# Kernel optimization log

Measured on AMD Instinct MI355X. Metric: run time of the kernel, lower is better.

## Reference

```python
import jax, jax.numpy as jnp
import numpy as np

B, N, H = 16, 1024, 4
CH = (64, 128, 256, 512)
KV = 960
EPS = 1e-5  # InstanceNorm2d default eps


def setup_inputs() -> dict:
    key = jax.random.key(0)
    ks = jax.random.split(key, 16)
    s = 0.02
    inp = {
        "emb1": jax.random.normal(ks[0], (B, N, CH[0]), jnp.float32),
        "emb2": jax.random.normal(ks[1], (B, N, CH[1]), jnp.float32),
        "emb3": jax.random.normal(ks[2], (B, N, CH[2]), jnp.float32),
        "emb4": jax.random.normal(ks[3], (B, N, CH[3]), jnp.float32),
        "emb_all": jax.random.normal(ks[4], (B, N, KV), jnp.float32),
        # per-head query weights (torch Linear weight layout [out, in])
        "Wq1": jax.random.normal(ks[5], (H, CH[0] // 4, CH[0] // 4), jnp.float32) * s,
        "Wq2": jax.random.normal(ks[6], (H, CH[1] // 4, CH[1] // 4), jnp.float32) * s,
        "Wq3": jax.random.normal(ks[7], (H, CH[2] // 4, CH[2] // 4), jnp.float32) * s,
        "Wq4": jax.random.normal(ks[8], (H, CH[3] // 4, CH[3] // 4), jnp.float32) * s,
        # NOTE: original forward only ever uses self.key[0] / self.value[0]
        "Wk": jax.random.normal(ks[9], (KV // 4, KV // 4), jnp.float32) * s,
        "Wv": jax.random.normal(ks[10], (KV // 4, KV // 4), jnp.float32) * s,
        "Wo1": jax.random.normal(ks[11], (CH[0], CH[0]), jnp.float32) * s,
        "Wo2": jax.random.normal(ks[12], (CH[1], CH[1]), jnp.float32) * s,
        "Wo3": jax.random.normal(ks[13], (CH[2], CH[2]), jnp.float32) * s,
        "Wo4": jax.random.normal(ks[14], (CH[3], CH[3]), jnp.float32) * s,
    }
    return inp


def _heads_from_all(x):
    # Reproduce the per-head channel regrouping of emb_all:
    # head h takes [16h:16(h+1)] of scale1, [32h:...] of scale2, etc. -> [B,H,N,240]
    b, n, _ = x.shape
    parts = [
        x[:, :, 0:64].reshape(b, n, H, 16),
        x[:, :, 64:192].reshape(b, n, H, 32),
        x[:, :, 192:448].reshape(b, n, H, 64),
        x[:, :, 448:960].reshape(b, n, H, 128),
    ]
    return jnp.concatenate(parts, axis=-1).transpose(0, 2, 1, 3)


def _scale_attn(emb, Wq, Wo, Kh, Vh):
    b, n, c = emb.shape
    d = c // H
    q = emb.reshape(b, n, H, d)
    # per-head linear (torch: x @ W.T): [B,H,N,d]
    Qh = jnp.einsum('bnhd,hed->bhne', q, Wq)
    # channel attention: Q^T K -> [B,H,d,240]
    scores = jnp.einsum('bhnd,bhnk->bhdk', Qh, Kh) / np.float32(np.sqrt(KV))
    # InstanceNorm2d over heads (per (b,h), normalize over last two dims, biased var)
    m = scores.mean(axis=(2, 3), keepdims=True)
    v = scores.var(axis=(2, 3), keepdims=True)
    probs = jax.nn.softmax((scores - m) / jnp.sqrt(v + EPS), axis=-1)
    # probs @ V^T -> [B,H,d,N]
    ctx = jnp.einsum('bhdk,bhnk->bhdn', probs, Vh)
    # permute(0,3,2,1) -> [B,N,d,H], flatten -> [B,N,c]
    ctx = ctx.transpose(0, 3, 2, 1).reshape(b, n, c)
    return jnp.einsum('bnc,ec->bne', ctx, Wo)


def reference(emb1, emb2, emb3, emb4, emb_all,
              Wq1, Wq2, Wq3, Wq4, Wk, Wv, Wo1, Wo2, Wo3, Wo4):
    heads = _heads_from_all(emb_all)  # [B,H,N,240]
    Kh = jnp.einsum('bhnd,ed->bhne', heads, Wk)
    Vh = jnp.einsum('bhnd,ed->bhne', heads, Wv)
    O1 = _scale_attn(emb1, Wq1, Wo1, Kh, Vh)
    O2 = _scale_attn(emb2, Wq2, Wo2, Kh, Vh)
    O3 = _scale_attn(emb3, Wq3, Wo3, Kh, Vh)
    O4 = _scale_attn(emb4, Wq4, Wo4, Kh, Vh)
    return (O1, O2, O3, O4)
```

## Files before the change

kernel.cpp:

```cpp
#include <hip/hip_runtime.h>
#include <hip/hip_bf16.h>
#include <math.h>

#define B_   16
#define N_   1024
#define H_   4
#define D240 240
#define SC_  57600

typedef unsigned short ushort;
typedef __attribute__((ext_vector_type(8))) short bf16x8;
typedef __attribute__((ext_vector_type(8))) unsigned short u16x8;
typedef __attribute__((ext_vector_type(4))) float f32x4;

__device__ __forceinline__ ushort f2b(float v) {
  __hip_bfloat16 h = __float2bfloat16(v);
  return *reinterpret_cast<ushort*>(&h);
}

__device__ __forceinline__ void gload16(const void* g, void* s) {
  __builtin_amdgcn_global_load_lds((const __attribute__((address_space(1))) void*)g,
                                   (__attribute__((address_space(3))) void*)s, 16, 0, 0);
}

__global__ __launch_bounds__(256) void conv_inputs(const float* __restrict__ emb_all,
                                                   const float* __restrict__ e1,
                                                   const float* __restrict__ e2,
                                                   const float* __restrict__ e3,
                                                   const float* __restrict__ e4,
                                                   ushort* __restrict__ heads,
                                                   ushort* __restrict__ embh) {
  const int t = threadIdx.x;
  const int which = t >> 7;
  const int gg = t & 127;
  const int h = gg >> 5;
  const int k0 = (gg & 31) * 8;
  const bool active = (k0 < 240);

  const float* base;
  int stride;
  long soff;
  if (which == 0) {
    base = emb_all; stride = 960;
    if (k0 < 16)       soff = h * 16 + k0;
    else if (k0 < 48)  soff = 64  + h * 32  + (k0 - 16);
    else if (k0 < 112) soff = 192 + h * 64  + (k0 - 48);
    else               soff = 448 + h * 128 + (k0 - 112);
  } else {
    if (k0 < 16)       { base = e1; stride = 64;  soff = h * 16  + k0; }
    else if (k0 < 48)  { base = e2; stride = 128; soff = h * 32  + (k0 - 16); }
    else if (k0 < 112) { base = e3; stride = 256; soff = h * 64  + (k0 - 48); }
    else               { base = e4; stride = 512; soff = h * 128 + (k0 - 112); }
  }
  ushort* dbase = which ? embh : heads;

  #pragma unroll
  for (int i = 0; i < 8; ++i) {
    const int bn = blockIdx.x * 8 + i;
    const int b = bn >> 10, n = bn & 1023;
    float4 p0 = {0.f, 0.f, 0.f, 0.f}, p1 = {0.f, 0.f, 0.f, 0.f};
    if (active) {
      const float* s = base + (long)bn * stride + soff;
      p0 = *(const float4*)s;
      p1 = *(const float4*)(s + 4);
    }
    u16x8 w;
    w[0] = f2b(p0.x); w[1] = f2b(p0.y); w[2] = f2b(p0.z); w[3] = f2b(p0.w);
    w[4] = f2b(p1.x); w[5] = f2b(p1.y); w[6] = f2b(p1.z); w[7] = f2b(p1.w);
    *(u16x8*)(dbase + (((long)b * H_ + h) * N_ + n) * 256 + k0) = w;
  }
}

__global__ __launch_bounds__(256) void conv_weights(
    const float* __restrict__ Wk, const float* __restrict__ Wv,
    const float* __restrict__ q1, const float* __restrict__ q2,
    const float* __restrict__ q3, const float* __restrict__ q4,
    const float* __restrict__ o1, const float* __restrict__ o2,
    const float* __restrict__ o3, const float* __restrict__ o4,
    ushort* __restrict__ wts) {
  long i = (long)blockIdx.x * 256 + threadIdx.x;
  if (i >= 716800) return;
  float v = 0.f;
  if (i < 122880) {
    const float* src = (i < 61440) ? Wk : Wv;
    long j = (i < 61440) ? i : i - 61440;
    int r = j / 256, k = j % 256;
    if (k < 240) v = src[(long)r * 240 + k];
  } else if (i < 368640) {
    long j = i - 122880;
    int h = j / 61440; int rem = j % 61440;
    int r = rem / 256, k = rem % 256;
    int s = r < 16 ? 0 : r < 48 ? 1 : r < 112 ? 2 : 3;
    const int dss[4] = {16, 32, 64, 128};
    const int qf[4]  = {0, 16, 48, 112};
    const float* qs[4] = {q1, q2, q3, q4};
    int d = dss[s], off = qf[s];
    if (k >= off && k < off + d)
      v = qs[s][((long)(h * d + (r - off))) * d + (k - off)];
  } else {
    long j = i - 368640;
    int s = j < 4096 ? 0 : j < 20480 ? 1 : j < 86016 ? 2 : 3;
    const long base[4] = {0, 4096, 20480, 86016};
    const int cs[4] = {64, 128, 256, 512};
    const float* os[4] = {o1, o2, o3, o4};
    long rem = j - base[s];
    int c = cs[s], d = c >> 2;
    int e = rem / c, kk = rem % c;
    v = os[s][(long)e * c + (kk % d) * 4 + kk / d];
  }
  wts[i] = f2b(v);
}

__device__ __forceinline__ void gemm_core_b16(
    ushort* As, ushort* Bs,
    const ushort* __restrict__ A, long lda,
    const ushort* __restrict__ Bm, long ldb,
    ushort* __restrict__ C, long ldc,
    int M, int Nn, int Npad, int K, int m0, int n0)
{
  const int tid = threadIdx.x;
  const int l = tid & 63, w = tid >> 6;
  const int wy = w >> 1, wx = w & 1;

  f32x4 acc[4][4];
  #pragma unroll
  for (int i = 0; i < 4; ++i)
    #pragma unroll
    for (int j = 0; j < 4; ++j) acc[i][j] = (f32x4)0.f;

  const int srow = tid >> 2;
  const int skc  = (tid & 3) * 8;
  int ra0 = m0 + srow;      ra0 = ra0 < M  ? ra0 : M - 1;
  int ra1 = m0 + srow + 64; ra1 = ra1 < M  ? ra1 : M - 1;
  int rb0 = n0 + srow;      rb0 = rb0 < Nn ? rb0 : Nn - 1;
  int rb1 = n0 + srow + 64; rb1 = rb1 < Nn ? rb1 : Nn - 1;
  const ushort* a0 = A  + (long)ra0 * lda + skc;
  const ushort* a1 = A  + (long)ra1 * lda + skc;
  const ushort* b0 = Bm + (long)rb0 * ldb + skc;
  const ushort* b1 = Bm + (long)rb1 * ldb + skc;
  ushort* lA0 = As + srow * 32 + skc;
  ushort* lA1 = As + (srow + 64) * 32 + skc;
  ushort* lB0 = Bs + srow * 32 + skc;
  ushort* lB1 = Bs + (srow + 64) * 32 + skc;

  const ushort* arp = As + (wy * 64 + (l & 15)) * 32 + (l >> 4) * 8;
  const ushort* brp = Bs + (wx * 64 + (l & 15)) * 32 + (l >> 4) * 8;

  for (int k0 = 0; k0 < K; k0 += 32) {
    __syncthreads();
    gload16(a0 + k0, lA0);
    gload16(a1 + k0, lA1);
    gload16(b0 + k0, lB0);
    gload16(b1 + k0, lB1);
    __syncthreads();
    bf16x8 af[4], bfr[4];
    #pragma unroll
    for (int i = 0; i < 4; ++i) af[i]  = *(const bf16x8*)(arp + i * 512);
    #pragma unroll
    for (int j = 0; j < 4; ++j) bfr[j] = *(const bf16x8*)(brp + j * 512);
    #pragma unroll
    for (int i = 0; i < 4; ++i)
      #pragma unroll
      for (int j = 0; j < 4; ++j)
        acc[i][j] = __builtin_amdgcn_mfma_f32_16x16x32_bf16(af[i], bfr[j], acc[i][j], 0, 0, 0);
  }

  const int quad = l >> 4, lc = l & 15;
  #pragma unroll
  for (int i = 0; i < 4; ++i) {
    #pragma unroll
    for (int r = 0; r < 4; ++r) {
      int row = m0 + wy * 64 + i * 16 + quad * 4 + r;
      if (row >= M) continue;
      ushort* Cr = C + (long)row * ldc;
      #pragma unroll
      for (int j = 0; j < 4; ++j) {
        int col = n0 + wx * 64 + j * 16 + lc;
        if (col < Nn) Cr[col] = f2b(acc[i][j][r]);
        else if (col < Npad) Cr[col] = 0;
      }
    }
  }
}

__global__ __launch_bounds__(256) void mfma_proj(
    const ushort* __restrict__ heads_b, const ushort* __restrict__ emb_h,
    const ushort* __restrict__ Wk_b, const ushort* __restrict__ Wv_b,
    const ushort* __restrict__ Wq_bd,
    ushort* __restrict__ Kh_T, ushort* __restrict__ Vh, ushort* __restrict__ Q_T)
{
  __shared__ __align__(16) ushort As[128 * 32];
  __shared__ __align__(16) ushort Bs[128 * 32];
  const int bx = blockIdx.x;
  const long sbh = 1024L * 256;

  if (bx < 1024) {
    const int bh = bx >> 4, t = bx & 15;
    gemm_core_b16(As, Bs,
                  Wk_b, 256,
                  heads_b + (long)bh * sbh, 256,
                  Kh_T + (long)bh * 240 * 1024, 1024,
                  240, 1024, 1024, 256, (t >> 3) * 128, (t & 7) * 128);
  } else if (bx < 2048) {
    const int local = bx - 1024;
    const int bh = local >> 4, t = local & 15;
    gemm_core_b16(As, Bs,
                  heads_b + (long)bh * sbh, 256,
                  Wv_b, 256,
                  Vh + (long)bh * sbh, 256,
                  1024, 240, 256, 256, (t >> 1) * 128, (t & 1) * 128);
  } else {
    const int local = bx - 2048;
    const int bh = local >> 4, t = local & 15;
    const int h = bh & 3;
    gemm_core_b16(As, Bs,
                  Wq_bd + h * 61440, 256,
                  emb_h + (long)bh * sbh, 256,
                  Q_T + (long)bh * 240 * 1024, 1024,
                  240, 1024, 1024, 256, (t >> 3) * 128, (t & 7) * 128);
  }
}

__global__ __launch_bounds__(256) void mfma_abT(
    const ushort* __restrict__ A, long lda, long AsY, long AsZ,
    const ushort* __restrict__ Bm, long ldb, long BsY, long BsZ,
    void* __restrict__ Cv, long ldc, long CsY, long CsZ,
    int M, int Nn, int Npad, int K, float alpha, int c_bf16, int tilesN)
{
  A  += blockIdx.y * AsY + blockIdx.z * AsZ;
  Bm += blockIdx.y * BsY + blockIdx.z * BsZ;

  const int m0 = (blockIdx.x / tilesN) * 128;
  const int n0 = (blockIdx.x % tilesN) * 128;
  const int tid = threadIdx.x;
  const int l = tid & 63, w = tid >> 6;
  const int wy = w >> 1, wx = w & 1;

  __shared__ __align__(16) ushort As[128 * 32];
  __shared__ __align__(16) ushort Bs[128 * 32];

  f32x4 acc[4][4];
  #pragma unroll
  for (int i = 0; i < 4; ++i)
    #pragma unroll
    for (int j = 0; j < 4; ++j) acc[i][j] = (f32x4)0.f;

  const int srow = tid >> 2;
  const int skc  = (tid & 3) * 8;
  int ra0 = m0 + srow;      ra0 = ra0 < M  ? ra0 : M - 1;
  int ra1 = m0 + srow + 64; ra1 = ra1 < M  ? ra1 : M - 1;
  int rb0 = n0 + srow;      rb0 = rb0 < Nn ? rb0 : Nn - 1;
  int rb1 = n0 + srow + 64; rb1 = rb1 < Nn ? rb1 : Nn - 1;
  const ushort* a0 = A  + (long)ra0 * lda + skc;
  const ushort* a1 = A  + (long)ra1 * lda + skc;
  const ushort* b0 = Bm + (long)rb0 * ldb + skc;
  const ushort* b1 = Bm + (long)rb1 * ldb + skc;
  ushort* lA0 = As + srow * 32 + skc;
  ushort* lA1 = As + (srow + 64) * 32 + skc;
  ushort* lB0 = Bs + srow * 32 + skc;
  ushort* lB1 = Bs + (srow + 64) * 32 + skc;

  const ushort* arp = As + (wy * 64 + (l & 15)) * 32 + (l >> 4) * 8;
  const ushort* brp = Bs + (wx * 64 + (l & 15)) * 32 + (l >> 4) * 8;

  for (int k0 = 0; k0 < K; k0 += 32) {
    __syncthreads();
    gload16(a0 + k0, lA0);
    gload16(a1 + k0, lA1);
    gload16(b0 + k0, lB0);
    gload16(b1 + k0, lB1);
    __syncthreads();
    bf16x8 af[4], bfr[4];
    #pragma unroll
    for (int i = 0; i < 4; ++i) af[i]  = *(const bf16x8*)(arp + i * 512);
    #pragma unroll
    for (int j = 0; j < 4; ++j) bfr[j] = *(const bf16x8*)(brp + j * 512);
    #pragma unroll
    for (int i = 0; i < 4; ++i)
      #pragma unroll
      for (int j = 0; j < 4; ++j)
        acc[i][j] = __builtin_amdgcn_mfma_f32_16x16x32_bf16(af[i], bfr[j], acc[i][j], 0, 0, 0);
  }

  const int quad = l >> 4, lc = l & 15;
  if (c_bf16) {
    ushort* C = (ushort*)Cv + blockIdx.y * CsY + blockIdx.z * CsZ;
    #pragma unroll
    for (int i = 0; i < 4; ++i) {
      #pragma unroll
      for (int r = 0; r < 4; ++r) {
        int row = m0 + wy * 64 + i * 16 + quad * 4 + r;
        if (row >= M) continue;
        ushort* Cr = C + (long)row * ldc;
        #pragma unroll
        for (int j = 0; j < 4; ++j) {
          int col = n0 + wx * 64 + j * 16 + lc;
          if (col < Nn) Cr[col] = f2b(acc[i][j][r] * alpha);
          else if (col < Npad) Cr[col] = 0;
        }
      }
    }
  } else {
    float* C = (float*)Cv + blockIdx.y * CsY + blockIdx.z * CsZ;
    #pragma unroll
    for (int i = 0; i < 4; ++i) {
      #pragma unroll
      for (int r = 0; r < 4; ++r) {
        int row = m0 + wy * 64 + i * 16 + quad * 4 + r;
        if (row >= M) continue;
        float* Cr = C + (long)row * ldc;
        #pragma unroll
        for (int j = 0; j < 4; ++j) {
          int col = n0 + wx * 64 + j * 16 + lc;
          if (col < Nn) Cr[col] = acc[i][j][r] * alpha;
        }
      }
    }
  }
}

__global__ __launch_bounds__(256) void mfma_ctx(const ushort* __restrict__ V,
                                                const ushort* __restrict__ P,
                                                ushort* __restrict__ ctx2) {
  const int h = blockIdx.y, b = blockIdx.z;
  const ushort* A  = V + (((long)b * H_ + h) * 1024) * 256;
  const ushort* Bm = P + (((long)b * H_ + h) * 240) * 256;

  const int m0 = (blockIdx.x >> 1) * 128;
  const int n0 = (blockIdx.x & 1) * 128;
  const int tid = threadIdx.x;
  const int l = tid & 63, w = tid >> 6;
  const int wy = w >> 1, wx = w & 1;

  __shared__ __align__(16) ushort As[128 * 32];
  __shared__ __align__(16) ushort Bs[128 * 32];

  f32x4 acc[4][4];
  #pragma unroll
  for (int i = 0; i < 4; ++i)
    #pragma unroll
    for (int j = 0; j < 4; ++j) acc[i][j] = (f32x4)0.f;

  const int srow = tid >> 2;
  const int skc  = (tid & 3) * 8;
  int rb0 = n0 + srow;      rb0 = rb0 < 240 ? rb0 : 239;
  int rb1 = n0 + srow + 64; rb1 = rb1 < 240 ? rb1 : 239;
  const ushort* a0 = A  + (long)(m0 + srow) * 256 + skc;
  const ushort* a1 = A  + (long)(m0 + srow + 64) * 256 + skc;
  const ushort* b0 = Bm + (long)rb0 * 256 + skc;
  const ushort* b1 = Bm + (long)rb1 * 256 + skc;
  ushort* lA0 = As + srow * 32 + skc;
  ushort* lA1 = As + (srow + 64) * 32 + skc;
  ushort* lB0 = Bs + srow * 32 + skc;
  ushort* lB1 = Bs + (srow + 64) * 32 + skc;

  const ushort* arp = As + (wy * 64 + (l & 15)) * 32 + (l >> 4) * 8;
  const ushort* brp = Bs + (wx * 64 + (l & 15)) * 32 + (l >> 4) * 8;

  for (int k0 = 0; k0 < 256; k0 += 32) {
    __syncthreads();
    gload16(a0 + k0, lA0);
    gload16(a1 + k0, lA1);
    gload16(b0 + k0, lB0);
    gload16(b1 + k0, lB1);
    __syncthreads();
    bf16x8 af[4], bfr[4];
    #pragma unroll
    for (int i = 0; i < 4; ++i) af[i]  = *(const bf16x8*)(arp + i * 512);
    #pragma unroll
    for (int j = 0; j < 4; ++j) bfr[j] = *(const bf16x8*)(brp + j * 512);
    #pragma unroll
    for (int i = 0; i < 4; ++i)
      #pragma unroll
      for (int j = 0; j < 4; ++j)
        acc[i][j] = __builtin_amdgcn_mfma_f32_16x16x32_bf16(af[i], bfr[j], acc[i][j], 0, 0, 0);
  }

  const int quad = l >> 4, lc = l & 15;
  const int dss[4] = {16, 32, 64, 128};
  const int qf[4]  = {0, 16, 48, 112};
  const int cf[4]  = {0, 64, 192, 448};
  #pragma unroll
  for (int i = 0; i < 4; ++i) {
    #pragma unroll
    for (int r = 0; r < 4; ++r) {
      int row = m0 + wy * 64 + i * 16 + quad * 4 + r;
      ushort* Cr = ctx2 + ((long)b * N_ + row) * 960;
      #pragma unroll
      for (int j = 0; j < 4; ++j) {
        int col = n0 + wx * 64 + j * 16 + lc;
        if (col < 240) {
          int s = col < 16 ? 0 : col < 48 ? 1 : col < 112 ? 2 : 3;
          int chan = cf[s] + h * dss[s] + (col - qf[s]);
          Cr[chan] = f2b(acc[i][j][r]);
        }
      }
    }
  }
}

__global__ __launch_bounds__(256) void mfma_oproj(const ushort* __restrict__ ctx2,
                                                  const ushort* __restrict__ Wo_b,
                                                  float* __restrict__ out) {
  const int bx = blockIdx.x;
  int s = bx < 128 ? 0 : bx < 256 ? 1 : bx < 512 ? 2 : 3;
  const int sbase[4] = {0, 128, 256, 512};
  const int cs_[4]   = {64, 128, 256, 512};
  const int coff_[4] = {0, 64, 192, 448};
  const int wo_[4]   = {0, 4096, 20480, 86016};
  const long oo_[4]  = {0, 1048576, 3145728, 7340032};
  const int c = cs_[s];
  const int nt = (c + 127) >> 7;
  const int local = bx - sbase[s];
  const int m0 = (local / nt) * 128;
  const int n0 = (local % nt) * 128;

  const ushort* A  = ctx2 + coff_[s];
  const ushort* Bm = Wo_b + wo_[s];
  float* C = out + oo_[s];
  const int K = c, Nn = c;

  const int tid = threadIdx.x;
  const int l = tid & 63, w = tid >> 6;
  const int wy = w >> 1, wx = w & 1;

  __shared__ __align__(16) ushort As[128 * 32];
  __shared__ __align__(16) ushort Bs[128 * 32];

  f32x4 acc[4][4];
  #pragma unroll
  for (int i = 0; i < 4; ++i)
    #pragma unroll
    for (int j = 0; j < 4; ++j) acc[i][j] = (f32x4)0.f;

  const int srow = tid >> 2;
  const int skc  = (tid & 3) * 8;
  int rb0 = n0 + srow;      rb0 = rb0 < Nn ? rb0 : Nn - 1;
  int rb1 = n0 + srow + 64; rb1 = rb1 < Nn ? rb1 : Nn - 1;
  const ushort* a0 = A  + (long)(m0 + srow) * 960 + skc;
  const ushort* a1 = A  + (long)(m0 + srow + 64) * 960 + skc;
  const ushort* b0 = Bm + (long)rb0 * c + skc;
  const ushort* b1 = Bm + (long)rb1 * c + skc;
  ushort* lA0 = As + srow * 32 + skc;
  ushort* lA1 = As + (srow + 64) * 32 + skc;
  ushort* lB0 = Bs + srow * 32 + skc;
  ushort* lB1 = Bs + (srow + 64) * 32 + skc;

  const ushort* arp = As + (wy * 64 + (l & 15)) * 32 + (l >> 4) * 8;
  const ushort* brp = Bs + (wx * 64 + (l & 15)) * 32 + (l >> 4) * 8;

  for (int k0 = 0; k0 < K; k0 += 32) {
    __syncthreads();
    gload16(a0 + k0, lA0);
    gload16(a1 + k0, lA1);
    gload16(b0 + k0, lB0);
    gload16(b1 + k0, lB1);
    __syncthreads();
    bf16x8 af[4], bfr[4];
    #pragma unroll
    for (int i = 0; i < 4; ++i) af[i]  = *(const bf16x8*)(arp + i * 512);
    #pragma unroll
    for (int j = 0; j < 4; ++j) bfr[j] = *(const bf16x8*)(brp + j * 512);
    #pragma unroll
    for (int i = 0; i < 4; ++i)
      #pragma unroll
      for (int j = 0; j < 4; ++j)
        acc[i][j] = __builtin_amdgcn_mfma_f32_16x16x32_bf16(af[i], bfr[j], acc[i][j], 0, 0, 0);
  }

  const int quad = l >> 4, lc = l & 15;
  #pragma unroll
  for (int i = 0; i < 4; ++i) {
    #pragma unroll
    for (int r = 0; r < 4; ++r) {
      int row = m0 + wy * 64 + i * 16 + quad * 4 + r;
      float* Cr = C + (long)row * c;
      #pragma unroll
      for (int j = 0; j < 4; ++j) {
        int col = n0 + wx * 64 + j * 16 + lc;
        if (col < Nn) Cr[col] = acc[i][j][r];
      }
    }
  }
}

__global__ __launch_bounds__(256) void in_stats(const float* __restrict__ sc0,
                                                const float* __restrict__ sc1,
                                                float* __restrict__ stats) {
  const int doffs[4] = {0, 16, 48, 112};
  const int dss[4]   = {16, 32, 64, 128};
  const int bh = blockIdx.x, sidx = blockIdx.y;
  const long base = (long)bh * SC_ + doffs[sidx] * D240;
  const float4* A4 = (const float4*)(sc0 + base);
  const float4* B4 = (const float4*)(sc1 + base);
  const int n4 = dss[sidx] * 60;

  float s = 0.f, s2 = 0.f;
  for (int i = threadIdx.x; i < n4; i += 256) {
    float4 a = A4[i], b = B4[i];
    float x0 = a.x + b.x, x1 = a.y + b.y, x2 = a.z + b.z, x3 = a.w + b.w;
    s  += x0 + x1 + x2 + x3;
    s2 += x0 * x0 + x1 * x1 + x2 * x2 + x3 * x3;
  }
  #pragma unroll
  for (int o = 32; o > 0; o >>= 1) { s += __shfl_down(s, o); s2 += __shfl_down(s2, o); }

  __shared__ float wsum[4], wsum2[4];
  const int wave = threadIdx.x >> 6, lane = threadIdx.x & 63;
  if (lane == 0) { wsum[wave] = s; wsum2[wave] = s2; }
  __syncthreads();
  if (threadIdx.x == 0) {
    float n = (float)(n4 * 4);
    float ts = wsum[0] + wsum[1] + wsum[2] + wsum[3];
    float ts2 = wsum2[0] + wsum2[1] + wsum2[2] + wsum2[3];
    float mean = ts / n;
    float var = ts2 / n - mean * mean;
    stats[(bh * 4 + sidx) * 2]     = mean;
    stats[(bh * 4 + sidx) * 2 + 1] = rsqrtf(var + 1e-5f);
  }
}

__global__ __launch_bounds__(256) void sm_apply(const float* __restrict__ sc0,
                                                const float* __restrict__ sc1,
                                                const float* __restrict__ stats,
                                                ushort* __restrict__ P) {
  const int bh = blockIdx.y;
  const int row = blockIdx.x * 4 + (threadIdx.x >> 6);
  const int lane = threadIdx.x & 63;
  const int s = row < 16 ? 0 : row < 48 ? 1 : row < 112 ? 2 : 3;
  const float mean = stats[(bh * 4 + s) * 2];
  const float rstd = stats[(bh * 4 + s) * 2 + 1];
  const long base = (long)bh * SC_ + (long)row * D240;
  const float* r0 = sc0 + base;
  const float* r1 = sc1 + base;
  ushort* p = P + ((long)bh * D240 + row) * 256;

  float v[4];
  float mx = -1e30f;
  #pragma unroll
  for (int j = 0; j < 4; ++j) {
    int c = lane + j * 64;
    v[j] = (c < D240) ? (r0[c] + r1[c] - mean) * rstd : -1e30f;
    mx = fmaxf(mx, v[j]);
  }
  #pragma unroll
  for (int o = 32; o > 0; o >>= 1) mx = fmaxf(mx, __shfl_xor(mx, o));
  float sum = 0.f;
  #pragma unroll
  for (int j = 0; j < 4; ++j) {
    int c = lane + j * 64;
    v[j] = (c < D240) ? __expf(v[j] - mx) : 0.f;
    sum += v[j];
  }
  #pragma unroll
  for (int o = 32; o > 0; o >>= 1) sum += __shfl_xor(sum, o);
  float inv = 1.f / sum;
  #pragma unroll
  for (int j = 0; j < 4; ++j) {
    int c = lane + j * 64;
    p[c] = (c < D240) ? f2b(v[j] * inv) : (ushort)0;
  }
}

extern "C" void kernel_launch(void* const* d_in, const int* in_sizes, int n_in,
                              void* d_out, int out_size, void* d_ws, size_t ws_size,
                              hipStream_t stream) {
  const float* emb[4] = {(const float*)d_in[0], (const float*)d_in[1],
                         (const float*)d_in[2], (const float*)d_in[3]};
  const float* emb_all = (const float*)d_in[4];
  const float* Wq[4] = {(const float*)d_in[5], (const float*)d_in[6],
                        (const float*)d_in[7], (const float*)d_in[8]};
  const float* Wk = (const float*)d_in[9];
  const float* Wv = (const float*)d_in[10];
  const float* Wo[4] = {(const float*)d_in[11], (const float*)d_in[12],
                        (const float*)d_in[13], (const float*)d_in[14]};
  float* out = (float*)d_out;
  float* sc0 = (float*)d_out;
  float* sc1 = (float*)d_out + 64L * SC_;

  ushort* wsb     = (ushort*)d_ws;
  ushort* heads_b = wsb;
  ushort* ctx2    = wsb;
  ushort* emb_h   = wsb + 16777216;
  ushort* P_b     = wsb + 16777216;
  ushort* Q_T     = wsb + 33554432;
  ushort* Kh_T    = wsb + 49283072;
  ushort* Vh      = wsb + 65011712;
  ushort* wts     = wsb + 81788928;
  ushort* Wk_b  = wts;
  ushort* Wv_b  = wts + 61440;
  ushort* Wq_bd = wts + 122880;
  ushort* Wo_b  = wts + 368640;
  float*  stats = (float*)(wsb + 82505728);

  const float alpha_s = 1.0f / sqrtf(960.0f);

  conv_weights<<<dim3(2800), 256, 0, stream>>>(Wk, Wv, Wq[0], Wq[1], Wq[2], Wq[3],
                                               Wo[0], Wo[1], Wo[2], Wo[3], wts);
  conv_inputs<<<dim3(2048), 256, 0, stream>>>(emb_all, emb[0], emb[1], emb[2], emb[3],
                                              heads_b, emb_h);

  mfma_proj<<<dim3(3072), 256, 0, stream>>>(heads_b, emb_h, Wk_b, Wv_b, Wq_bd,
                                            Kh_T, Vh, Q_T);

  mfma_abT<<<dim3(4, 64, 2), 256, 0, stream>>>(
      Q_T, 1024, 240L * 1024, 512,
      Kh_T, 1024, 240L * 1024, 512,
      sc0, 240, (long)SC_, 64L * SC_,
      240, 240, 240, 512, alpha_s, 0, 2);

  in_stats<<<dim3(64, 4), 256, 0, stream>>>(sc0, sc1, stats);
  sm_apply<<<dim3(60, 64), 256, 0, stream>>>(sc0, sc1, stats, P_b);

  mfma_ctx<<<dim3(16, H_, B_), 256, 0, stream>>>(Vh, P_b, ctx2);

  mfma_oproj<<<dim3(1024), 256, 0, stream>>>(ctx2, Wo_b, out);
}
```

Measured before the change: 349.7 us.

## Fuse fp32-to-bf16 input conversion and head regrouping into projection GEMM

Removes the separate conv_inputs kernel and its bf16 staging buffers. The projection GEMM now reads fp32 activations directly, applies the per-head channel gather, converts to bf16 in registers and writes the result into LDS, prefetching the next k-slice into registers. This saves a full write and read of the staged bf16 inputs and one launch. In exchange, emb_all is now read and converted twice (for K and V) and once per tile column, and the loads are strided fp32 instead of async LDS loads.

Result: no change. 346.8 us (-0.8%).

```diff
diff --git a/kernel.cpp b/kernel.cpp
--- a/kernel.cpp
+++ b/kernel.cpp
@@ -23,52 +23,11 @@
                                    (__attribute__((address_space(3))) void*)s, 16, 0, 0);
 }
 
-__global__ __launch_bounds__(256) void conv_inputs(const float* __restrict__ emb_all,
-                                                   const float* __restrict__ e1,
-                                                   const float* __restrict__ e2,
-                                                   const float* __restrict__ e3,
-                                                   const float* __restrict__ e4,
-                                                   ushort* __restrict__ heads,
-                                                   ushort* __restrict__ embh) {
-  const int t = threadIdx.x;
-  const int which = t >> 7;
-  const int gg = t & 127;
-  const int h = gg >> 5;
-  const int k0 = (gg & 31) * 8;
-  const bool active = (k0 < 240);
-
-  const float* base;
-  int stride;
-  long soff;
-  if (which == 0) {
-    base = emb_all; stride = 960;
-    if (k0 < 16)       soff = h * 16 + k0;
-    else if (k0 < 48)  soff = 64  + h * 32  + (k0 - 16);
-    else if (k0 < 112) soff = 192 + h * 64  + (k0 - 48);
-    else               soff = 448 + h * 128 + (k0 - 112);
-  } else {
-    if (k0 < 16)       { base = e1; stride = 64;  soff = h * 16  + k0; }
-    else if (k0 < 48)  { base = e2; stride = 128; soff = h * 32  + (k0 - 16); }
-    else if (k0 < 112) { base = e3; stride = 256; soff = h * 64  + (k0 - 48); }
-    else               { base = e4; stride = 512; soff = h * 128 + (k0 - 112); }
-  }
-  ushort* dbase = which ? embh : heads;
-
-  #pragma unroll
-  for (int i = 0; i < 8; ++i) {
-    const int bn = blockIdx.x * 8 + i;
-    const int b = bn >> 10, n = bn & 1023;
-    float4 p0 = {0.f, 0.f, 0.f, 0.f}, p1 = {0.f, 0.f, 0.f, 0.f};
-    if (active) {
-      const float* s = base + (long)bn * stride + soff;
-      p0 = *(const float4*)s;
-      p1 = *(const float4*)(s + 4);
-    }
-    u16x8 w;
-    w[0] = f2b(p0.x); w[1] = f2b(p0.y); w[2] = f2b(p0.z); w[3] = f2b(p0.w);
-    w[4] = f2b(p1.x); w[5] = f2b(p1.y); w[6] = f2b(p1.z); w[7] = f2b(p1.w);
-    *(u16x8*)(dbase + (((long)b * H_ + h) * N_ + n) * 256 + k0) = w;
-  }
+__device__ __forceinline__ u16x8 cvt8(float4 a, float4 b) {
+  u16x8 w;
+  w[0] = f2b(a.x); w[1] = f2b(a.y); w[2] = f2b(a.z); w[3] = f2b(a.w);
+  w[4] = f2b(b.x); w[5] = f2b(b.y); w[6] = f2b(b.z); w[7] = f2b(b.w);
+  return w;
 }
 
 __global__ __launch_bounds__(256) void conv_weights(
@@ -111,47 +70,105 @@
   wts[i] = f2b(v);
 }
 
-__device__ __forceinline__ void gemm_core_b16(
-    ushort* As, ushort* Bs,
-    const ushort* __restrict__ A, long lda,
-    const ushort* __restrict__ Bm, long ldb,
-    ushort* __restrict__ C, long ldc,
-    int M, int Nn, int Npad, int K, int m0, int n0)
+__global__ __launch_bounds__(256) void mfma_proj(
+    const float* __restrict__ emb_all,
+    const float* __restrict__ e1, const float* __restrict__ e2,
+    const float* __restrict__ e3, const float* __restrict__ e4,
+    const ushort* __restrict__ Wk_b, const ushort* __restrict__ Wv_b,
+    const ushort* __restrict__ Wq_bd,
+    ushort* __restrict__ Kh_T, ushort* __restrict__ Vh, ushort* __restrict__ Q_T)
 {
+  __shared__ __align__(16) ushort As[128 * 32];
+  __shared__ __align__(16) ushort Bs[128 * 32];
+
+  const int bx = blockIdx.x;
+  const int mode = bx < 1024 ? 0 : bx < 2048 ? 1 : 2;
+  const int local = bx - (mode == 0 ? 0 : mode == 1 ? 1024 : 2048);
+  const int bh = local >> 4, t16 = local & 15;
+  const int b = bh >> 2, h = bh & 3;
+
+  int m0, n0;
+  const ushort* W;
+  ushort* C; long ldc; int M, Nn, Npad;
+  if (mode == 0) {
+    m0 = (t16 >> 3) * 128; n0 = (t16 & 7) * 128;
+    W = Wk_b; C = Kh_T + (long)bh * 240 * 1024; ldc = 1024;
+    M = 240; Nn = 1024; Npad = 1024;
+  } else if (mode == 1) {
+    m0 = (t16 >> 1) * 128; n0 = (t16 & 1) * 128;
+    W = Wv_b; C = Vh + (long)bh * 1024 * 256; ldc = 256;
+    M = 1024; Nn = 240; Npad = 256;
+  } else {
+    m0 = (t16 >> 3) * 128; n0 = (t16 & 7) * 128;
+    W = Wq_bd + h * 61440; C = Q_T + (long)bh * 240 * 1024; ldc = 1024;
+    M = 240; Nn = 1024; Npad = 1024;
+  }
+  const bool wa = (mode != 1);
+  const int wbase = wa ? m0 : n0;
+  const int cbase = wa ? n0 : m0;
+
   const int tid = threadIdx.x;
   const int l = tid & 63, w = tid >> 6;
   const int wy = w >> 1, wx = w & 1;
-
-  f32x4 acc[4][4];
-  #pragma unroll
-  for (int i = 0; i < 4; ++i)
-    #pragma unroll
-    for (int j = 0; j < 4; ++j) acc[i][j] = (f32x4)0.f;
-
   const int srow = tid >> 2;
   const int skc  = (tid & 3) * 8;
-  int ra0 = m0 + srow;      ra0 = ra0 < M  ? ra0 : M - 1;
-  int ra1 = m0 + srow + 64; ra1 = ra1 < M  ? ra1 : M - 1;
-  int rb0 = n0 + srow;      rb0 = rb0 < Nn ? rb0 : Nn - 1;
-  int rb1 = n0 + srow + 64; rb1 = rb1 < Nn ? rb1 : Nn - 1;
-  const ushort* a0 = A  + (long)ra0 * lda + skc;
-  const ushort* a1 = A  + (long)ra1 * lda + skc;
-  const ushort* b0 = Bm + (long)rb0 * ldb + skc;
-  const ushort* b1 = Bm + (long)rb1 * ldb + skc;
-  ushort* lA0 = As + srow * 32 + skc;
-  ushort* lA1 = As + (srow + 64) * 32 + skc;
-  ushort* lB0 = Bs + srow * 32 + skc;
-  ushort* lB1 = Bs + (srow + 64) * 32 + skc;
+
+  int wr0 = wbase + srow;      wr0 = wr0 < 240 ? wr0 : 239;
+  int wr1 = wbase + srow + 64; wr1 = wr1 < 240 ? wr1 : 239;
+  const ushort* w0p = W + (long)wr0 * 256 + skc;
+  const ushort* w1p = W + (long)wr1 * 256 + skc;
+  ushort* Ws = wa ? As : Bs;
+  ushort* Cs = wa ? Bs : As;
+  ushort* lW0 = Ws + srow * 32 + skc;
+  ushort* lW1 = Ws + (srow + 64) * 32 + skc;
+  ushort* lC0 = Cs + srow * 32 + skc;
+  ushort* lC1 = Cs + (srow + 64) * 32 + skc;
+
+  const long rowb0 = (long)(b * 1024 + cbase + srow);
+  const long rowb1 = rowb0 + 64;
+
+  auto ldconv = [&](int k, float4 f[4]) {
+    f[0] = f[1] = f[2] = f[3] = make_float4(0.f, 0.f, 0.f, 0.f);
+    if (k < 240) {
+      const float* base; long str, off;
+      if (mode == 2) {
+        if (k < 16)       { base = e1; str = 64;  off = h * 16  + k; }
+        else if (k < 48)  { base = e2; str = 128; off = h * 32  + (k - 16); }
+        else if (k < 112) { base = e3; str = 256; off = h * 64  + (k - 48); }
+        else              { base = e4; str = 512; off = h * 128 + (k - 112); }
+      } else {
+        base = emb_all; str = 960;
+        if (k < 16)       off = h * 16 + k;
+        else if (k < 48)  off = 64  + h * 32  + (k - 16);
+        else if (k < 112) off = 192 + h * 64  + (k - 48);
+        else              off = 448 + h * 128 + (k - 112);
+      }
+      const float* s0 = base + rowb0 * str + off;
+      const float* s1 = base + rowb1 * str + off;
+      f[0] = *(const float4*)s0; f[1] = *(const float4*)(s0 + 4);
+      f[2] = *(const float4*)s1; f[3] = *(const float4*)(s1 + 4);
+    }
+  };
+
+  f32x4 acc[4][4];
+  #pragma unroll
+  for (int i = 0; i < 4; ++i)
+    #pragma unroll
+    for (int j = 0; j < 4; ++j) acc[i][j] = (f32x4)0.f;
 
   const ushort* arp = As + (wy * 64 + (l & 15)) * 32 + (l >> 4) * 8;
   const ushort* brp = Bs + (wx * 64 + (l & 15)) * 32 + (l >> 4) * 8;
 
-  for (int k0 = 0; k0 < K; k0 += 32) {
-    __syncthreads();
-    gload16(a0 + k0, lA0);
-    gload16(a1 + k0, lA1);
-    gload16(b0 + k0, lB0);
-    gload16(b1 + k0, lB1);
+  float4 f[4];
+  ldconv(skc, f);
+
+  for (int k0 = 0; k0 < 256; k0 += 32) {
+    __syncthreads();
+    gload16(w0p + k0, lW0);
+    gload16(w1p + k0, lW1);
+    *(u16x8*)lC0 = cvt8(f[0], f[1]);
+    *(u16x8*)lC1 = cvt8(f[2], f[3]);
+    if (k0 + 32 < 256) ldconv(k0 + 32 + skc, f);
     __syncthreads();
     bf16x8 af[4], bfr[4];
     #pragma unroll
@@ -180,44 +197,6 @@
         else if (col < Npad) Cr[col] = 0;
       }
     }
-  }
-}
-
-__global__ __launch_bounds__(256) void mfma_proj(
-    const ushort* __restrict__ heads_b, const ushort* __restrict__ emb_h,
-    const ushort* __restrict__ Wk_b, const ushort* __restrict__ Wv_b,
-    const ushort* __restrict__ Wq_bd,
-    ushort* __restrict__ Kh_T, ushort* __restrict__ Vh, ushort* __restrict__ Q_T)
-{
-  __shared__ __align__(16) ushort As[128 * 32];
-  __shared__ __align__(16) ushort Bs[128 * 32];
-  const int bx = blockIdx.x;
-  const long sbh = 1024L * 256;
-
-  if (bx < 1024) {
-    const int bh = bx >> 4, t = bx & 15;
-    gemm_core_b16(As, Bs,
-                  Wk_b, 256,
-                  heads_b + (long)bh * sbh, 256,
-                  Kh_T + (long)bh * 240 * 1024, 1024,
-                  240, 1024, 1024, 256, (t >> 3) * 128, (t & 7) * 128);
-  } else if (bx < 2048) {
-    const int local = bx - 1024;
-    const int bh = local >> 4, t = local & 15;
-    gemm_core_b16(As, Bs,
-                  heads_b + (long)bh * sbh, 256,
-                  Wv_b, 256,
-                  Vh + (long)bh * sbh, 256,
-                  1024, 240, 256, 256, (t >> 1) * 128, (t & 1) * 128);
-  } else {
-    const int local = bx - 2048;
-    const int bh = local >> 4, t = local & 15;
-    const int h = bh & 3;
-    gemm_core_b16(As, Bs,
-                  Wq_bd + h * 61440, 256,
-                  emb_h + (long)bh * sbh, 256,
-                  Q_T + (long)bh * 240 * 1024, 1024,
-                  240, 1024, 1024, 256, (t >> 3) * 128, (t & 7) * 128);
   }
 }
 
@@ -578,15 +557,13 @@
   float* sc0 = (float*)d_out;
   float* sc1 = (float*)d_out + 64L * SC_;
 
-  ushort* wsb     = (ushort*)d_ws;
-  ushort* heads_b = wsb;
-  ushort* ctx2    = wsb;
-  ushort* emb_h   = wsb + 16777216;
-  ushort* P_b     = wsb + 16777216;
-  ushort* Q_T     = wsb + 33554432;
-  ushort* Kh_T    = wsb + 49283072;
-  ushort* Vh      = wsb + 65011712;
-  ushort* wts     = wsb + 81788928;
+  ushort* wsb   = (ushort*)d_ws;
+  ushort* P_b   = wsb;
+  ushort* ctx2  = wsb + 4194304;
+  ushort* Q_T   = wsb + 33554432;
+  ushort* Kh_T  = wsb + 49283072;
+  ushort* Vh    = wsb + 65011712;
+  ushort* wts   = wsb + 81788928;
   ushort* Wk_b  = wts;
   ushort* Wv_b  = wts + 61440;
   ushort* Wq_bd = wts + 122880;
@@ -597,11 +574,9 @@
 
   conv_weights<<<dim3(2800), 256, 0, stream>>>(Wk, Wv, Wq[0], Wq[1], Wq[2], Wq[3],
                                                Wo[0], Wo[1], Wo[2], Wo[3], wts);
-  conv_inputs<<<dim3(2048), 256, 0, stream>>>(emb_all, emb[0], emb[1], emb[2], emb[3],
-                                              heads_b, emb_h);
-
-  mfma_proj<<<dim3(3072), 256, 0, stream>>>(heads_b, emb_h, Wk_b, Wv_b, Wq_bd,
-                                            Kh_T, Vh, Q_T);
+
+  mfma_proj<<<dim3(3072), 256, 0, stream>>>(emb_all, emb[0], emb[1], emb[2], emb[3],
+                                            Wk_b, Wv_b, Wq_bd, Kh_T, Vh, Q_T);
 
   mfma_abT<<<dim3(4, 64, 2), 256, 0, stream>>>(
       Q_T, 1024, 240L * 1024, 512,
```
